# Optimization experiments

Measured on AMD Instinct MI355X. Metric: run time of the kernel, lower is better.

Reference implementation:

```python
import jax, jax.numpy as jnp
import numpy as np

C = 256
HEADS = 8
WIN = 8
SHIFT = 4
HIDDEN = int(C * 4.0)
EPS = 1e-6


def setup_inputs() -> dict:
    key = jax.random.key(0)
    ks = jax.random.split(key, 16)
    s = lambda fan: 1.0 / np.sqrt(fan)
    return {
        "x": jax.random.normal(ks[0], (16, C, 64, 64), jnp.float32),
        "norm1_g": jnp.ones((C,), jnp.float32),
        "norm1_b": jnp.zeros((C,), jnp.float32),
        "in_w": jax.random.normal(ks[1], (3 * C, C), jnp.float32) * s(C),
        "in_b": jnp.zeros((3 * C,), jnp.float32),
        "out_w": jax.random.normal(ks[2], (C, C), jnp.float32) * s(C),
        "out_b": jnp.zeros((C,), jnp.float32),
        "proj_w": jax.random.normal(ks[3], (C, C), jnp.float32) * s(C),
        "proj_b": jnp.zeros((C,), jnp.float32),
        "norm2_g": jnp.ones((C,), jnp.float32),
        "norm2_b": jnp.zeros((C,), jnp.float32),
        "fc1_w": jax.random.normal(ks[4], (HIDDEN, C), jnp.float32) * s(C),
        "fc1_b": jnp.zeros((HIDDEN,), jnp.float32),
        "fc2_w": jax.random.normal(ks[5], (C, HIDDEN), jnp.float32) * s(HIDDEN),
        "fc2_b": jnp.zeros((C,), jnp.float32),
    }


def _ln2d(x, g, b):
    # LayerNorm over channel dim of NCHW (equivalent to permute->LN->permute)
    mu = jnp.mean(x, axis=1, keepdims=True)
    var = jnp.mean(jnp.square(x - mu), axis=1, keepdims=True)
    xh = (x - mu) * jax.lax.rsqrt(var + EPS)
    return xh * g[None, :, None, None] + b[None, :, None, None]


def _window_partition(x, win):
    b, c, h, w = x.shape
    x = x.reshape(b, c, h // win, win, w // win, win)
    x = jnp.transpose(x, (0, 2, 4, 3, 5, 1))
    return x.reshape(-1, win * win, c)


def _window_reverse(windows, win, h, w, b):
    c = windows.shape[-1]
    x = windows.reshape(b, h // win, w // win, win, win, c)
    x = jnp.transpose(x, (0, 5, 1, 3, 2, 4))
    return x.reshape(b, c, h, w)


def _mha(x, in_w, in_b, out_w, out_b):
    # x: [nW, L, C]; standard nn.MultiheadAttention math (batch_first)
    nw, L, c = x.shape
    dh = c // HEADS
    qkv = x @ in_w.T + in_b  # [nW, L, 3C]
    q, k, v = jnp.split(qkv, 3, axis=-1)
    reshape_h = lambda t: t.reshape(nw, L, HEADS, dh).transpose(0, 2, 1, 3)
    q, k, v = reshape_h(q), reshape_h(k), reshape_h(v)
    scores = jnp.einsum("nhid,nhjd->nhij", q, k) / jnp.sqrt(jnp.float32(dh)).astype(x.dtype)
    attn = jax.nn.softmax(scores, axis=-1)
    out = jnp.einsum("nhij,nhjd->nhid", attn, v)
    out = out.transpose(0, 2, 1, 3).reshape(nw, L, c)
    return out @ out_w.T + out_b


def reference(x, norm1_g, norm1_b, in_w, in_b, out_w, out_b, proj_w, proj_b,
              norm2_g, norm2_b, fc1_w, fc1_b, fc2_w, fc2_b):
    shortcut = x
    xn = _ln2d(x, norm1_g, norm1_b)
    b, c, h, w = xn.shape
    win = min(WIN, h, w)
    pad_h = (win - h % win) % win
    pad_w = (win - w % win) % win
    if pad_h or pad_w:
        xn = jnp.pad(xn, ((0, 0), (0, 0), (0, pad_h), (0, pad_w)))
    hp, wp = xn.shape[2], xn.shape[3]
    shifted = 0 < SHIFT < win
    if shifted:
        xn = jnp.roll(xn, shift=(-SHIFT, -SHIFT), axis=(2, 3))
    windows = _window_partition(xn, win)
    attn_out = _mha(windows, in_w, in_b, out_w, out_b)
    attn_out = attn_out @ proj_w.T + proj_b
    y = _window_reverse(attn_out, win, hp, wp, b)
    if shifted:
        y = jnp.roll(y, shift=(SHIFT, SHIFT), axis=(2, 3))
    if pad_h or pad_w:
        y = y[:, :, :h, :w]
    y = shortcut + y
    # MLP: 1x1 convs = per-pixel linear layers, exact GELU (torch default)
    z = _ln2d(y, norm2_g, norm2_b)
    z = jnp.einsum("bchw,oc->bohw", z, fc1_w) + fc1_b[None, :, None, None]
    z = jax.nn.gelu(z, approximate=False)
    z = jnp.einsum("bchw,oc->bohw", z, fc2_w) + fc2_b[None, :, None, None]
    return y + z
```

## Files before the change

### kernel.cpp

```cpp
#include <hip/hip_runtime.h>

typedef unsigned short u16;
typedef unsigned int   u32;
typedef __bf16 bf16_t;
typedef bf16_t bf16x8 __attribute__((ext_vector_type(8)));
typedef float  f32x4  __attribute__((ext_vector_type(4)));

__device__ __forceinline__ float b2f(u16 u) {
  union { float f; u32 i; } v; v.i = ((u32)u) << 16; return v.f;
}
__device__ __forceinline__ u16 f2b(float f) {
  union { float f; u32 i; } v; v.f = f;
  u32 r = v.i + 0x7FFFu + ((v.i >> 16) & 1u);
  return (u16)(r >> 16);
}
__device__ __forceinline__ void ld4(const float* p, float* o) {
  const float4 v = *(const float4*)p; o[0]=v.x; o[1]=v.y; o[2]=v.z; o[3]=v.w;
}
__device__ __forceinline__ void ld4(const u16* p, float* o) {
  union { ushort4 v; u16 e[4]; } u; u.v = *(const ushort4*)p;
#pragma unroll
  for (int k = 0; k < 4; ++k) o[k] = b2f(u.e[k]);
}

__device__ __forceinline__ void gld16(const u16* g, u16* l) {
  __builtin_amdgcn_global_load_lds(
      (const __attribute__((address_space(1))) void*)g,
      (__attribute__((address_space(3))) void*)l, 16, 0, 0);
}

__device__ __forceinline__ float fast_gelu(float v) {
  const float u = v * 0.7071067811865475f;
  const float s = fabsf(u);
  const float t = __builtin_amdgcn_rcpf(fmaf(0.3275911f, s, 1.f));
  const float poly = t*(0.254829592f + t*(-0.284496736f +
                     t*(1.421413741f + t*(-1.453152027f + t*1.061405429f))));
  const float E = exp2f(-s*s*1.4426950408889634f);
  const float q = poly * E;
  const float phi = (u >= 0.f) ? (2.f - q) : q;
  return 0.5f * v * phi;
}

__global__ void conv_w(const float* __restrict__ src, u16* __restrict__ dst, int n) {
  const int i = blockIdx.x * 256 + threadIdx.x;
  if (i < n) dst[i] = f2b(src[i]);
}

__global__ void prep_w2(const float* __restrict__ proj_w, const float* __restrict__ out_w,
                        u16* __restrict__ W2) {
  const int o = blockIdx.x, c = threadIdx.x;
  float acc = 0.f;
  for (int m = 0; m < 256; ++m)
    acc += proj_w[o*256 + m] * out_w[m*256 + c];
  W2[o*256 + c] = f2b(acc);
}

__global__ void prep_b2(const float* __restrict__ proj_w, const float* __restrict__ out_b,
                        const float* __restrict__ proj_b, float* __restrict__ b2v) {
  const int o = threadIdx.x;
  float acc = proj_b[o];
  for (int m = 0; m < 256; ++m) acc += proj_w[o*256 + m] * out_b[m];
  b2v[o] = acc;
}

__global__ __launch_bounds__(256, 2)
void ln1_kernel(const float* __restrict__ x, const float* __restrict__ g,
                const float* __restrict__ bb, u16* __restrict__ xn_tok,
                u16* __restrict__ x_tok) {
  const int bx = blockIdx.x;
  const int h = bx >> 1, w0 = (bx & 1) << 5;
  const int b = blockIdx.y;
  const int tid = threadIdx.x;
  __shared__ float X[256][33];
  __shared__ float ps[8][32], pq[8][32];
  __shared__ float mu_s[32], rs_s[32];
  const int w = tid & 31, cg = tid >> 5;
  float sum = 0.f, sq = 0.f;
  const float* xb = x + ((size_t)b * 256) * 4096 + h * 64 + w0;
  for (int i = 0; i < 32; ++i) {
    const int c = i*8 + cg;
    const float v = xb[(size_t)c * 4096 + w];
    X[c][w] = v; sum += v; sq += v*v;
  }
  ps[cg][w] = sum; pq[cg][w] = sq;
  __syncthreads();
  if (tid < 32) {
    float s = 0.f, q2 = 0.f;
#pragma unroll
    for (int j = 0; j < 8; ++j) { s += ps[j][tid]; q2 += pq[j][tid]; }
    const float mu = s * (1.f/256.f);
    mu_s[tid] = mu;
    rs_s[tid] = rsqrtf(fmaxf(q2 * (1.f/256.f) - mu*mu, 0.f) + 1e-6f);
  }
  __syncthreads();
  const int c = tid;
  const float gc = g[c], bc = bb[c];
  const int hp = (h + 60) & 63;
  const int wi = hp >> 3, tr = hp & 7;
  const int tokb = (b << 6) + (wi << 3);
  for (int w2 = 0; w2 < 32; ++w2) {
    const int wp = (w0 + w2 + 60) & 63;
    const int tok = (tokb + (wp >> 3)) * 64 + tr*8 + (wp & 7);
    const float v = X[c][w2];
    xn_tok[(size_t)tok * 256 + c] = f2b((v - mu_s[w2]) * rs_s[w2] * gc + bc);
    x_tok [(size_t)tok * 256 + c] = f2b(v);
  }
}

constexpr int EPI_BIAS = 0, EPI_GELU = 1, EPI_RES = 2;

template<int N, int K, int NB, int EPI, typename OutT, typename ResT>
__global__ __launch_bounds__(256, 2)
void gemm_bt(const u16* __restrict__ A, const u16* __restrict__ W,
             const float* __restrict__ bias, const ResT* __restrict__ res,
             OutT* __restrict__ C) {
  __shared__ u16 SMEM[2*128*64];
  u16* As = SMEM;
  u16* Ws = SMEM + 8192;
  const int tid = threadIdx.x;
  const int lane = tid & 63;
  const int wave = tid >> 6;
  const int wm = (wave >> 1) << 6;
  const int wn = (wave & 1) << 6;
  const int id = blockIdx.x;
  const int kk = id >> 3, xx = id & 7;
  const int bn = kk % NB;
  const int bm = (kk / NB) * 8 + xx;
  const u16* Ab = A + (size_t)bm * 128 * K;
  const u16* Wb = W + (size_t)bn * 128 * K;
  f32x4 acc[4][4] = {};

  const int srl = lane >> 3;
  const int sp  = lane & 7;
  auto stage = [&](int kb) {
#pragma unroll
    for (int e = 0; e < 4; ++e) {
      const int r = (wave*4 + e)*8 + srl;
      const int c = sp ^ (r & 7);
      const int lo = (wave*4 + e)*512;
      gld16(Ab + (size_t)r*K + kb + c*8, As + lo);
      gld16(Wb + (size_t)r*K + kb + c*8, Ws + lo);
    }
  };

  for (int kc = 0; kc < K/64; ++kc) {
    stage(kc*64);
    __syncthreads();
#pragma unroll
    for (int ks = 0; ks < 2; ++ks) {
      bf16x8 af[4], wf[4];
#pragma unroll
      for (int i = 0; i < 4; ++i) {
        const int ra = wm + i*16 + (lane & 15);
        const int pa = ((ks<<2) + (lane >> 4)) ^ (ra & 7);
        af[i] = *(const bf16x8*)(As + ra*64 + pa*8);
        const int rb = wn + i*16 + (lane & 15);
        const int pb = ((ks<<2) + (lane >> 4)) ^ (rb & 7);
        wf[i] = *(const bf16x8*)(Ws + rb*64 + pb*8);
      }
#pragma unroll
      for (int i = 0; i < 4; ++i)
#pragma unroll
        for (int j = 0; j < 4; ++j)
          acc[i][j] = __builtin_amdgcn_mfma_f32_16x16x32_bf16(af[i], wf[j], acc[i][j], 0, 0, 0);
    }
    __syncthreads();
  }
  float* Es = (float*)SMEM + wave * (16*68);
  const int c0 = lane & 15, g4 = lane >> 4;
  float bj[4];
#pragma unroll
  for (int j = 0; j < 4; ++j) bj[j] = bias[bn*128 + wn + j*16 + c0];
#pragma unroll
  for (int i = 0; i < 4; ++i) {
#pragma unroll
    for (int j = 0; j < 4; ++j)
#pragma unroll
      for (int r = 0; r < 4; ++r) {
        float v = acc[i][j][r] + bj[j];
        if constexpr (EPI == EPI_GELU) v = fast_gelu(v);
        Es[(g4*4 + r)*68 + j*16 + c0] = v;
      }
#pragma unroll
    for (int t = 0; t < 2; ++t) {
      const int r16 = t*8 + (lane >> 3);
      const int cc = (lane & 7) * 8;
      const float* ep = Es + r16*68 + cc;
      float v[8];
#pragma unroll
      for (int k = 0; k < 8; ++k) v[k] = ep[k];
      const int row = bm*128 + wm + i*16 + r16;
      const int colg = bn*128 + wn + cc;
      if constexpr (EPI == EPI_RES) {
        float rv[8];
        ld4(res + (size_t)row * N + colg, rv);
        ld4(res + (size_t)row * N + colg + 4, rv + 4);
#pragma unroll
        for (int k = 0; k < 8; ++k) v[k] += rv[k];
      }
      if constexpr (sizeof(OutT) == 2) {
        union { uint4 q; u16 e[8]; } ov;
#pragma unroll
        for (int k = 0; k < 8; ++k) ov.e[k] = f2b(v[k]);
        *(uint4*)((u16*)C + (size_t)row * N + colg) = ov.q;
      } else {
        float4 o0 = {v[0],v[1],v[2],v[3]}, o1 = {v[4],v[5],v[6],v[7]};
        float* cp = (float*)C + (size_t)row * N + colg;
        *(float4*)cp = o0; *(float4*)(cp + 4) = o1;
      }
    }
  }
}

__global__ __launch_bounds__(256, 2)
void attn_kernel(const u16* __restrict__ qkv, u16* __restrict__ attn) {
  const int h = blockIdx.x;
  const int n = blockIdx.y;
  const int tid = threadIdx.x;
  const int lane = tid & 63, wv = tid >> 6;
  __shared__ u16 Qs[64*40];
  __shared__ u16 Ks[64*40];
  __shared__ u16 Vt[32*72];
  __shared__ u16 Ps[64*72];
  {
    const int row = tid >> 2, ch = tid & 3;
    const u16* base = qkv + (size_t)(n*64 + row) * 768 + h*32 + ch*8;
    *(uint4*)(Qs + row*40 + ch*8) = *(const uint4*)(base);
    *(uint4*)(Ks + row*40 + ch*8) = *(const uint4*)(base + 256);
    union { uint4 v; u16 e[8]; } tmp;
    tmp.v = *(const uint4*)(base + 512);
#pragma unroll
    for (int j = 0; j < 8; ++j) Vt[(ch*8 + j)*72 + row] = tmp.e[j];
  }
  __syncthreads();
  const int mrow = (wv << 4) + (lane & 15);
  const int q4 = lane >> 4;
  f32x4 s[4];
  {
    bf16x8 qa = *(const bf16x8*)(Qs + mrow*40 + q4*8);
#pragma unroll
    for (int nt = 0; nt < 4; ++nt) {
      bf16x8 kb = *(const bf16x8*)(Ks + (nt*16 + (lane & 15))*40 + q4*8);
      f32x4 z = {0.f, 0.f, 0.f, 0.f};
      s[nt] = __builtin_amdgcn_mfma_f32_16x16x32_bf16(qa, kb, z, 0, 0, 0);
    }
  }
  float pr[4][4];
#pragma unroll
  for (int r = 0; r < 4; ++r) {
    float m0 = fmaxf(fmaxf(s[0][r], s[1][r]), fmaxf(s[2][r], s[3][r]));
    m0 = fmaxf(m0, __shfl_xor(m0, 1, 64));
    m0 = fmaxf(m0, __shfl_xor(m0, 2, 64));
    m0 = fmaxf(m0, __shfl_xor(m0, 4, 64));
    m0 = fmaxf(m0, __shfl_xor(m0, 8, 64));
    const float cs = 0.25500526571944696f;
    float p0 = exp2f(fminf((s[0][r] - m0) * cs, 0.f));
    float p1 = exp2f(fminf((s[1][r] - m0) * cs, 0.f));
    float p2 = exp2f(fminf((s[2][r] - m0) * cs, 0.f));
    float p3 = exp2f(fminf((s[3][r] - m0) * cs, 0.f));
    float sum = p0 + p1 + p2 + p3;
    sum += __shfl_xor(sum, 1, 64);
    sum += __shfl_xor(sum, 2, 64);
    sum += __shfl_xor(sum, 4, 64);
    sum += __shfl_xor(sum, 8, 64);
    const float inv = 1.f / sum;
    pr[0][r] = p0*inv; pr[1][r] = p1*inv; pr[2][r] = p2*inv; pr[3][r] = p3*inv;
  }
  {
    const int c = lane & 15;
#pragma unroll
    for (int nt = 0; nt < 4; ++nt)
#pragma unroll
      for (int r = 0; r < 4; ++r)
        Ps[((wv<<4) + (q4<<2) + r)*72 + nt*16 + c] = f2b(pr[nt][r]);
  }
  __syncthreads();
  f32x4 o0 = {0.f,0.f,0.f,0.f}, o1 = {0.f,0.f,0.f,0.f};
#pragma unroll
  for (int ks = 0; ks < 2; ++ks) {
    bf16x8 pa = *(const bf16x8*)(Ps + mrow*72 + ks*32 + q4*8);
    bf16x8 v0 = *(const bf16x8*)(Vt + (lane & 15)*72 + ks*32 + q4*8);
    bf16x8 v1 = *(const bf16x8*)(Vt + (16 + (lane & 15))*72 + ks*32 + q4*8);
    o0 = __builtin_amdgcn_mfma_f32_16x16x32_bf16(pa, v0, o0, 0, 0, 0);
    o1 = __builtin_amdgcn_mfma_f32_16x16x32_bf16(pa, v1, o1, 0, 0, 0);
  }
  {
    u16* Os = Qs + wv * 640;
    const int c = lane & 15;
#pragma unroll
    for (int r = 0; r < 4; ++r) {
      Os[((q4<<2) + r)*40 + c]      = f2b(o0[r]);
      Os[((q4<<2) + r)*40 + 16 + c] = f2b(o1[r]);
    }
    const int rr = lane >> 2, d0 = (lane & 3) * 8;
    union { uint4 q; u16 e[8]; } ov;
#pragma unroll
    for (int k = 0; k < 8; ++k) ov.e[k] = Os[rr*40 + d0 + k];
    *(uint4*)(attn + (size_t)(n*64 + (wv<<4) + rr) * 256 + h*32 + d0) = ov.q;
  }
}

template<typename YT>
__global__ __launch_bounds__(256, 4)
void ln2_kernel(const YT* __restrict__ y, const float* __restrict__ g,
                const float* __restrict__ bb, u16* __restrict__ zn) {
  const int t = blockIdx.x * 4 + (threadIdx.x >> 6);
  const int lane = threadIdx.x & 63;
  float f[4];
  ld4(y + (size_t)t*256 + lane*4, f);
  float sum = f[0]+f[1]+f[2]+f[3];
  float sq  = f[0]*f[0]+f[1]*f[1]+f[2]*f[2]+f[3]*f[3];
#pragma unroll
  for (int d = 32; d; d >>= 1) { sum += __shfl_xor(sum, d, 64); sq += __shfl_xor(sq, d, 64); }
  const float mu = sum * (1.f/256.f);
  const float rs = rsqrtf(fmaxf(sq * (1.f/256.f) - mu*mu, 0.f) + 1e-6f);
  const float4 gv = *(const float4*)(g + lane*4);
  const float4 bv = *(const float4*)(bb + lane*4);
  union { ushort4 v; u16 e[4]; } ov;
  ov.e[0] = f2b((f[0]-mu)*rs*gv.x + bv.x);
  ov.e[1] = f2b((f[1]-mu)*rs*gv.y + bv.y);
  ov.e[2] = f2b((f[2]-mu)*rs*gv.z + bv.z);
  ov.e[3] = f2b((f[3]-mu)*rs*gv.w + bv.w);
  *(ushort4*)(zn + (size_t)t*256 + lane*4) = ov.v;
}

__global__ __launch_bounds__(256, 2)
void scatter_kernel(const float* __restrict__ z, float* __restrict__ out) {
  __shared__ float T[64 * 260];
  const int bx = blockIdx.x;
  const int b = bx >> 6, h = bx & 63;
  const int tid = threadIdx.x;
  const int hp = (h + 60) & 63;
  const int wi = hp >> 3, tr = hp & 7;
  const int base = (b*64 + wi*8)*64 + tr*8;
  const int c0 = (tid & 63) * 4;
#pragma unroll
  for (int p = 0; p < 16; ++p) {
    const int r = p*4 + (tid >> 6);
    const int t = base + (r >> 3)*64 + (r & 7);
    const float4 v = *(const float4*)(z + (size_t)t*256 + c0);
    *(float4*)(T + ((r + 4) & 63)*260 + c0) = v;
  }
  __syncthreads();
  float* ob = out + (size_t)b*1048576 + (size_t)h*64;
#pragma unroll
  for (int p = 0; p < 16; ++p) {
    const int c = p*16 + (tid >> 6)*4 + ((tid & 63) >> 4);
    const int w4 = (tid & 15) * 4;
    float4 v;
    v.x = T[(w4+0)*260 + c];
    v.y = T[(w4+1)*260 + c];
    v.z = T[(w4+2)*260 + c];
    v.w = T[(w4+3)*260 + c];
    *(float4*)(ob + (size_t)c*4096 + w4) = v;
  }
}

extern "C" void kernel_launch(void* const* d_in, const int* in_sizes, int n_in,
                              void* d_out, int out_size, void* d_ws, size_t ws_size,
                              hipStream_t stream) {
  const float* x       = (const float*)d_in[0];
  const float* norm1_g = (const float*)d_in[1];
  const float* norm1_b = (const float*)d_in[2];
  const float* in_w    = (const float*)d_in[3];
  const float* in_b    = (const float*)d_in[4];
  const float* out_w   = (const float*)d_in[5];
  const float* out_b   = (const float*)d_in[6];
  const float* proj_w  = (const float*)d_in[7];
  const float* proj_b  = (const float*)d_in[8];
  const float* norm2_g = (const float*)d_in[9];
  const float* norm2_b = (const float*)d_in[10];
  const float* fc1_w   = (const float*)d_in[11];
  const float* fc1_b   = (const float*)d_in[12];
  const float* fc2_w   = (const float*)d_in[13];
  const float* fc2_b   = (const float*)d_in[14];
  float* out = (float*)d_out;

  const size_t nA = 16777216;
  const size_t nH = 8388608;

  char* base = (char*)d_ws;
  const bool yf32 = ws_size >= (14*nA + 1573888 + 1024);

  u16*   B  = (u16*)base;
  u16*   Cb = (u16*)(base + nA*2);
  u16*   H1 = (u16*)(base + nA*2);
  float* Z  = (float*)(base + nA*6);
  u16*   A  = (u16*)(base + nA*8);
  char*  Dp = base + nA*10;
  char*  Wp = Dp + (yf32 ? nA*4 : nA*2);
  u16* W2    = (u16*)Wp;
  u16* inw_h = W2 + 65536;
  u16* fc1_h = inw_h + 196608;
  u16* fc2_h = fc1_h + 262144;
  float* b2v = (float*)(fc2_h + 262144);

  conv_w<<<768, 256, 0, stream>>>(in_w, inw_h, 196608);
  conv_w<<<1024, 256, 0, stream>>>(fc1_w, fc1_h, 262144);
  conv_w<<<1024, 256, 0, stream>>>(fc2_w, fc2_h, 262144);
  prep_w2<<<256, 256, 0, stream>>>(proj_w, out_w, W2);
  prep_b2<<<1, 256, 0, stream>>>(proj_w, out_b, proj_b, b2v);

  ln1_kernel<<<dim3(128, 16), 256, 0, stream>>>(x, norm1_g, norm1_b, B, A);
  gemm_bt<768, 256, 6, EPI_BIAS, u16, u16>
      <<<3072, 256, 0, stream>>>(B, inw_h, in_b, nullptr, Cb);
  attn_kernel<<<dim3(8, 1024), 256, 0, stream>>>(Cb, B);
  if (yf32) {
    float* D = (float*)Dp;
    gemm_bt<256, 256, 2, EPI_RES, float, u16>
        <<<1024, 256, 0, stream>>>(B, W2, b2v, A, D);
    ln2_kernel<float><<<16384, 256, 0, stream>>>(D, norm2_g, norm2_b, B);
    for (int mh = 0; mh < 2; ++mh) {
      gemm_bt<1024, 256, 8, EPI_GELU, u16, u16>
          <<<2048, 256, 0, stream>>>(B + mh*nH, fc1_h, fc1_b, nullptr, H1);
      gemm_bt<256, 1024, 2, EPI_RES, float, float>
          <<<512, 256, 0, stream>>>(H1, fc2_h, fc2_b, D + mh*nH, Z + mh*nH);
    }
  } else {
    u16* D = (u16*)Dp;
    gemm_bt<256, 256, 2, EPI_RES, u16, u16>
        <<<1024, 256, 0, stream>>>(B, W2, b2v, A, D);
    ln2_kernel<u16><<<16384, 256, 0, stream>>>(D, norm2_g, norm2_b, B);
    for (int mh = 0; mh < 2; ++mh) {
      gemm_bt<1024, 256, 8, EPI_GELU, u16, u16>
          <<<2048, 256, 0, stream>>>(B + mh*nH, fc1_h, fc1_b, nullptr, H1);
      gemm_bt<256, 1024, 2, EPI_RES, float, u16>
          <<<512, 256, 0, stream>>>(H1, fc2_h, fc2_b, (u16*)Dp + mh*nH, Z + mh*nH);
    }
  }
  scatter_kernel<<<1024, 256, 0, stream>>>(Z, out);
}
```

Baseline: 432.4 us.

## Load GEMM MFMA fragments directly from global memory, dropping LDS staging

The GEMM kernel no longer stages A and W tiles into shared memory with global_load_lds and barriers. Each wave now reads its bf16x8 MFMA fragments straight from global memory in a fully unrolled K loop, and shared memory is kept only for the epilogue. The launch-bounds occupancy hint goes from 2 to 3 blocks. This removes the LDS round trip and the per-chunk syncthreads, but it loses sharing of tiles across waves, so each fragment is fetched redundantly through L1/L2 with strided row accesses. The full unroll also raises register pressure.

```diff
diff --git a/kernel.cpp b/kernel.cpp
--- a/kernel.cpp
+++ b/kernel.cpp
@@ -21,12 +21,6 @@
   union { ushort4 v; u16 e[4]; } u; u.v = *(const ushort4*)p;
 #pragma unroll
   for (int k = 0; k < 4; ++k) o[k] = b2f(u.e[k]);
-}
-
-__device__ __forceinline__ void gld16(const u16* g, u16* l) {
-  __builtin_amdgcn_global_load_lds(
-      (const __attribute__((address_space(1))) void*)g,
-      (__attribute__((address_space(3))) void*)l, 16, 0, 0);
 }
 
 __device__ __forceinline__ float fast_gelu(float v) {
@@ -110,13 +104,11 @@
 constexpr int EPI_BIAS = 0, EPI_GELU = 1, EPI_RES = 2;
 
 template<int N, int K, int NB, int EPI, typename OutT, typename ResT>
-__global__ __launch_bounds__(256, 2)
+__global__ __launch_bounds__(256, 3)
 void gemm_bt(const u16* __restrict__ A, const u16* __restrict__ W,
              const float* __restrict__ bias, const ResT* __restrict__ res,
              OutT* __restrict__ C) {
-  __shared__ u16 SMEM[2*128*64];
-  u16* As = SMEM;
-  u16* Ws = SMEM + 8192;
+  __shared__ float EsM[4][16*68];
   const int tid = threadIdx.x;
   const int lane = tid & 63;
   const int wave = tid >> 6;
@@ -126,37 +118,20 @@
   const int kk = id >> 3, xx = id & 7;
   const int bn = kk % NB;
   const int bm = (kk / NB) * 8 + xx;
-  const u16* Ab = A + (size_t)bm * 128 * K;
-  const u16* Wb = W + (size_t)bn * 128 * K;
+  const int r15 = lane & 15, quad = lane >> 4;
+  const u16* Ab = A + (size_t)(bm*128 + wm + r15) * K + quad*8;
+  const u16* Wb = W + (size_t)(bn*128 + wn + r15) * K + quad*8;
   f32x4 acc[4][4] = {};
 
-  const int srl = lane >> 3;
-  const int sp  = lane & 7;
-  auto stage = [&](int kb) {
-#pragma unroll
-    for (int e = 0; e < 4; ++e) {
-      const int r = (wave*4 + e)*8 + srl;
-      const int c = sp ^ (r & 7);
-      const int lo = (wave*4 + e)*512;
-      gld16(Ab + (size_t)r*K + kb + c*8, As + lo);
-      gld16(Wb + (size_t)r*K + kb + c*8, Ws + lo);
-    }
-  };
-
-  for (int kc = 0; kc < K/64; ++kc) {
-    stage(kc*64);
-    __syncthreads();
+#pragma unroll
+  for (int kb = 0; kb < K; kb += 64) {
 #pragma unroll
     for (int ks = 0; ks < 2; ++ks) {
       bf16x8 af[4], wf[4];
 #pragma unroll
       for (int i = 0; i < 4; ++i) {
-        const int ra = wm + i*16 + (lane & 15);
-        const int pa = ((ks<<2) + (lane >> 4)) ^ (ra & 7);
-        af[i] = *(const bf16x8*)(As + ra*64 + pa*8);
-        const int rb = wn + i*16 + (lane & 15);
-        const int pb = ((ks<<2) + (lane >> 4)) ^ (rb & 7);
-        wf[i] = *(const bf16x8*)(Ws + rb*64 + pb*8);
+        af[i] = *(const bf16x8*)(Ab + (size_t)i*16*K + kb + ks*32);
+        wf[i] = *(const bf16x8*)(Wb + (size_t)i*16*K + kb + ks*32);
       }
 #pragma unroll
       for (int i = 0; i < 4; ++i)
@@ -164,9 +139,9 @@
         for (int j = 0; j < 4; ++j)
           acc[i][j] = __builtin_amdgcn_mfma_f32_16x16x32_bf16(af[i], wf[j], acc[i][j], 0, 0, 0);
     }
-    __syncthreads();
-  }
-  float* Es = (float*)SMEM + wave * (16*68);
+  }
+
+  float* Es = EsM[wave];
   const int c0 = lane & 15, g4 = lane >> 4;
   float bj[4];
 #pragma unroll
```

Result: slower. 643.3 us (+48.7%).
